# Optimization experiments

Hardware: AMD Instinct MI355X
Metric: run time of the kernel (lower is better)

Reference implementation:

```python
import jax, jax.numpy as jnp
import numpy as np

T, B, XIN, H, A = 4096, 1024, 2, 16, 4


def setup_inputs() -> dict:
    key = jax.random.key(0)
    ks = jax.random.split(key, 16)
    inp = {
        "x": jax.random.normal(ks[0], (T * B, XIN), dtype=jnp.float32),
        "done": jax.random.randint(ks[1], (T * B,), 0, 2, dtype=jnp.int32),
        "action": jax.random.randint(ks[2], (T * B,), 0, A, dtype=jnp.int32),
        "h0": jax.random.normal(ks[3], (B, H), dtype=jnp.float32) * 0.1,
        "c0": jax.random.normal(ks[4], (B, H), dtype=jnp.float32) * 0.1,
        # MLP: Linear(XIN, 16) (orthogonal init approximated by scaled normal)
        "w1": jax.random.normal(ks[5], (H, XIN), dtype=jnp.float32) * (1.0 / np.sqrt(XIN)),
        "b1": jnp.zeros((H,), dtype=jnp.float32),
        # LSTM(16, 16): gate order i, f, g, o (PyTorch convention)
        "w_ih": jax.random.normal(ks[6], (4 * H, H), dtype=jnp.float32) * (1.0 / np.sqrt(H)),
        "w_hh": jax.random.normal(ks[7], (4 * H, H), dtype=jnp.float32) * (1.0 / np.sqrt(H)),
        "b_ih": jnp.zeros((4 * H,), dtype=jnp.float32),
        "b_hh": jnp.zeros((4 * H,), dtype=jnp.float32),
        "actor_w": jax.random.normal(ks[8], (A, H), dtype=jnp.float32) * 0.01,
        "actor_b": jnp.zeros((A,), dtype=jnp.float32),
        "critic_w": jax.random.normal(ks[9], (1, H), dtype=jnp.float32) * (1.0 / np.sqrt(H)),
        "critic_b": jnp.zeros((1,), dtype=jnp.float32),
    }
    return inp


def reference(x, done, action, h0, c0, w1, b1, w_ih, w_hh, b_ih, b_hh,
              actor_w, actor_b, critic_w, critic_b):
    # MLP encoder: Linear(XIN,16) + ReLU, then reshape to [T, B, 16]
    hid = jax.nn.relu(x @ w1.T + b1)
    hid = hid.reshape(-1, h0.shape[0], H)          # [T, B, H]
    done_f = done.reshape(-1, h0.shape[0]).astype(hid.dtype)  # [T, B]

    def step(carry, inp):
        h, c = carry
        xt, dt = inp
        m = (1.0 - dt)[:, None]                    # reset mask per env
        h = h * m
        c = c * m
        gates = xt @ w_ih.T + b_ih + h @ w_hh.T + b_hh   # [B, 4H]
        i, f, g, o = jnp.split(gates, 4, axis=-1)
        i = jax.nn.sigmoid(i)
        f = jax.nn.sigmoid(f)
        g = jnp.tanh(g)
        o = jax.nn.sigmoid(o)
        c = f * c + i * g
        h = o * jnp.tanh(c)
        return (h, c), h

    (hN, cN), hs = jax.lax.scan(step, (h0, c0), (hid, done_f))
    hidden = hs.reshape(-1, H)                     # [T*B, H]

    logits = hidden @ actor_w.T + actor_b          # [T*B, A]
    logp_all = jax.nn.log_softmax(logits, axis=-1)
    logp = jnp.take_along_axis(logp_all, action[:, None].astype(jnp.int32), axis=1)[:, 0]
    entropy = -jnp.sum(jnp.exp(logp_all) * logp_all, axis=-1)
    value = (hidden @ critic_w.T + critic_b)[:, 0]
    return action, logp, entropy, value, hN, cN
```

## Files before the change

### kernel.cpp

```cpp
#include <hip/hip_runtime.h>

#define TT 4096
#define BB 1024
#define LCH 5
#define CH 32
#define NC 128
#define TB 4194304
#define OFF_LOGP (TB)
#define OFF_ENT  (2*TB)
#define OFF_VAL  (3*TB)
#define OFF_HN   (4*TB)
#define OFF_CN   (4*TB + 16384)

#define NL2E  (-1.4426950408889634f)
#define N2L2E (-2.8853900817779268f)

typedef float    f32x2 __attribute__((ext_vector_type(2)));
typedef float    f32x4 __attribute__((ext_vector_type(4)));
typedef _Float16 f16x4 __attribute__((ext_vector_type(4)));

__device__ __forceinline__ float fexp2(float x){
#if __has_builtin(__builtin_amdgcn_exp2f)
    return __builtin_amdgcn_exp2f(x);
#else
    return __expf(x * 0.6931471805599453f);
#endif
}

__device__ __forceinline__ float fsig(float x){
    return __builtin_amdgcn_rcpf(1.f + __expf(-x));
}
__device__ __forceinline__ float ftanh_(float x){
    return 1.f - 2.f*__builtin_amdgcn_rcpf(1.f + __expf(2.f*x));
}
__device__ __forceinline__ f16x4 to_h4(f32x4 v){
    f16x4 r;
    r[0]=(_Float16)v[0]; r[1]=(_Float16)v[1]; r[2]=(_Float16)v[2]; r[3]=(_Float16)v[3];
    return r;
}
__device__ __forceinline__ f32x4 from_h4(f16x4 v){
    f32x4 r;
    r[0]=(float)v[0]; r[1]=(float)v[1]; r[2]=(float)v[2]; r[3]=(float)v[3];
    return r;
}
__device__ __forceinline__ f32x4 mfma16(f16x4 a, f16x4 b, f32x4 c){
    return __builtin_amdgcn_mfma_f32_16x16x16f16(a, b, c, 0, 0, 0);
}

#define KPARAMS const float* __restrict__ x, const int* __restrict__ done, \
    const int* __restrict__ action, const float* __restrict__ h0, \
    const float* __restrict__ c0, const float* __restrict__ w1, \
    const float* __restrict__ b1, const float* __restrict__ w_ih, \
    const float* __restrict__ w_hh, const float* __restrict__ bsum, \
    const float* __restrict__ bsum_s, const float* __restrict__ wih_s, \
    const float* __restrict__ whh_s, const float* __restrict__ hw16, \
    const float* __restrict__ actor_w, const float* __restrict__ actor_b, \
    const float* __restrict__ critic_w, const float* __restrict__ critic_b, \
    float* __restrict__ out, float* __restrict__ carry, int* __restrict__ valid

#define KARGS x,done,action,h0,c0,w1,b1,w_ih,w_hh,bsum,bsum_s,wih_s,whh_s,hw16,actor_w,actor_b,critic_w,critic_b,out,carry,valid

struct Frags {
    f16x4 wih[4], whh[4], hw;
    f32x4 biasC[4], biasH;
    f32x2 w1r[4];
    f32x4 b1r;
};

__device__ __forceinline__ void load_frags(Frags& F, int lo, int hi,
    const float* w1, const float* b1, const float* wih_s, const float* whh_s,
    const float* bsum_s, const float* hw16, const float* actor_b,
    const float* critic_b)
{
#pragma unroll
    for (int mt = 0; mt < 4; mt++) {
        F.wih[mt]   = to_h4(*(const f32x4*)(wih_s + (16*mt+lo)*16 + 4*hi));
        F.whh[mt]   = to_h4(*(const f32x4*)(whh_s + (16*mt+lo)*16 + 4*hi));
        F.biasC[mt] = *(const f32x4*)(bsum_s + 16*mt + 4*hi);
    }
    F.hw = to_h4(*(const f32x4*)(hw16 + lo*16 + 4*hi));
    if (hi == 0)       F.biasH = *(const f32x4*)(actor_b);
    else if (hi == 1)  F.biasH = (f32x4){critic_b[0], 0.f, 0.f, 0.f};
    else               F.biasH = (f32x4){0.f, 0.f, 0.f, 0.f};
#pragma unroll
    for (int r = 0; r < 4; r++) {
        F.w1r[r] = *(const f32x2*)(w1 + (4*hi+r)*2);
        F.b1r[r] = b1[4*hi+r];
    }
}

__device__ __forceinline__ void step_mfma(const Frags& F, f16x4& hh, f32x4& cc,
    f32x2 xv, int a, int idx, bool do_store, int hi, float* __restrict__ out)
{
    f32x4 hid;
#pragma unroll
    for (int r = 0; r < 4; r++)
        hid[r] = fmaxf(fmaf(F.w1r[r][0], xv[0], fmaf(F.w1r[r][1], xv[1], F.b1r[r])), 0.f);
    f16x4 hidh = to_h4(hid);
    f32x4 g0 = mfma16(F.whh[0], hh, F.biasC[0]);
    f32x4 g1 = mfma16(F.whh[1], hh, F.biasC[1]);
    f32x4 g2 = mfma16(F.whh[2], hh, F.biasC[2]);
    f32x4 g3 = mfma16(F.whh[3], hh, F.biasC[3]);
    g0 = mfma16(F.wih[0], hidh, g0);
    g1 = mfma16(F.wih[1], hidh, g1);
    g2 = mfma16(F.wih[2], hidh, g2);
    g3 = mfma16(F.wih[3], hidh, g3);
    f32x4 o4, cv4;
#pragma unroll
    for (int r = 0; r < 4; r++) {
        float A0 = 1.f + fexp2(g0[r]);
        float A1 = 1.f + fexp2(g1[r]);
        float A2 = 1.f + fexp2(g2[r]);
        float A3 = 1.f + fexp2(g3[r]);
        float R01 = __builtin_amdgcn_rcpf(A0*A1);
        float R23 = __builtin_amdgcn_rcpf(A2*A3);
        float si = A1*R01;
        float sf = A0*R01;
        float tg = fmaf(2.f, A3*R23, -1.f);
        o4[r]    = A2*R23;
        cv4[r]   = fmaf(sf, cc[r], si*tg);
    }
    cc = cv4;
    float B0 = 1.f + fexp2(N2L2E*cv4[0]);
    float B1 = 1.f + fexp2(N2L2E*cv4[1]);
    float B2 = 1.f + fexp2(N2L2E*cv4[2]);
    float B3 = 1.f + fexp2(N2L2E*cv4[3]);
    float Ra = __builtin_amdgcn_rcpf(B0*B1);
    float Rb = __builtin_amdgcn_rcpf(B2*B3);
    f32x4 hn;
    hn[0] = o4[0]*fmaf(2.f, B1*Ra, -1.f);
    hn[1] = o4[1]*fmaf(2.f, B0*Ra, -1.f);
    hn[2] = o4[2]*fmaf(2.f, B3*Rb, -1.f);
    hn[3] = o4[3]*fmaf(2.f, B2*Rb, -1.f);
    hh = to_h4(hn);
    f32x4 dh = mfma16(F.hw, hh, F.biasH);
    if (do_store) {
        if (hi == 0) {
            float e0 = __expf(dh[0]), e1 = __expf(dh[1]);
            float e2 = __expf(dh[2]), e3 = __expf(dh[3]);
            float s  = e0+e1+e2+e3;
            float ls = __logf(s);
            float t  = e0*dh[0] + e1*dh[1] + e2*dh[2] + e3*dh[3];
            float ent = ls - t*__builtin_amdgcn_rcpf(s);
            float lsel = (a==0) ? dh[0] : (a==1) ? dh[1] : (a==2) ? dh[2] : dh[3];
            out[idx]            = (float)a;
            out[OFF_LOGP + idx] = lsel - ls;
            out[OFF_ENT  + idx] = ent;
        } else if (hi == 1) {
            out[OFF_VAL + idx] = dh[0];
        }
    }
}

__global__ __launch_bounds__(256) __attribute__((amdgpu_waves_per_eu(4, 8)))
void k_phase1(KPARAMS)
{
    const int tid  = blockIdx.x*256 + threadIdx.x;
    const int lane = tid & 63;
    const int lo = lane & 15, hi = lane >> 4;
    const int w    = tid >> 6;
    const int ch   = w >> 6;
    const int base = (w & 63) << 4;
    const int b    = base + lo;
    const int t0   = ch << LCH;

    Frags F;
    load_frags(F, lo, hi, w1, b1, wih_s, whh_s, bsum_s, hw16, actor_b, critic_b);

    f16x4 hh = {(_Float16)0.f,(_Float16)0.f,(_Float16)0.f,(_Float16)0.f};
    f32x4 cc = {0.f,0.f,0.f,0.f};
    int hr = 0;

    int   d_cur = done[t0*BB + b];
    f32x2 x_cur = *(const f32x2*)(x + 2*(size_t)(t0*BB + b));
    int   a_cur = action[t0*BB + b];

#pragma unroll 2
    for (int s = 0; s < CH; s++) {
        const int idx = (t0 + s)*BB + b;
        const int   d  = d_cur;
        const f32x2 xv = x_cur;
        const int   a  = a_cur;
        if (s + 1 < CH) {
            d_cur = done[idx + BB];
            x_cur = *(const f32x2*)(x + 2*(size_t)(idx + BB));
            a_cur = action[idx + BB];
        }
        hr |= d;
        if (d) {
            hh = (f16x4){(_Float16)0.f,(_Float16)0.f,(_Float16)0.f,(_Float16)0.f};
            cc = (f32x4){0.f,0.f,0.f,0.f};
        }
        step_mfma(F, hh, cc, xv, a, idx, true, hi, out);
    }
    if (hr) {
        f32x4 hf = from_h4(hh);
#pragma unroll
        for (int r = 0; r < 4; r++) {
            carry[(ch*32 + 4*hi + r)*BB + b]      = hf[r];
            carry[(ch*32 + 16 + 4*hi + r)*BB + b] = cc[r];
        }
    }
    if (hi == 0) valid[ch*BB + b] = hr;
}

__global__ __launch_bounds__(256) __attribute__((amdgpu_waves_per_eu(4, 8)))
void k_phase2(KPARAMS)
{
    const int tid  = blockIdx.x*256 + threadIdx.x;
    const int lane = tid & 63;
    const int lo = lane & 15, hi = lane >> 4;
    const int w    = tid >> 6;
    const int ch   = w >> 6;
    const int base = (w & 63) << 4;
    const int b    = base + lo;
    const int t0   = ch << LCH;

    Frags F;
    load_frags(F, lo, hi, w1, b1, wih_s, whh_s, bsum_s, hw16, actor_b, critic_b);

    f32x4 hf, cc;
    bool active;
    if (ch == 0) {
        hf = *(const f32x4*)(h0 + b*16 + 4*hi);
        cc = *(const f32x4*)(c0 + b*16 + 4*hi);
        active = true;
    } else {
        active = (valid[(ch-1)*BB + b] != 0);
#pragma unroll
        for (int r = 0; r < 4; r++) {
            hf[r] = carry[((ch-1)*32 + 4*hi + r)*BB + b];
            cc[r] = carry[((ch-1)*32 + 16 + 4*hi + r)*BB + b];
        }
    }
    f16x4 hh = to_h4(hf);

    for (int s = 0; s < CH; s++) {
        if (!__ballot(active)) break;
        const int idx = (t0 + s)*BB + b;
        const int d = done[idx];
        if (d) active = false;
        const f32x2 xv = *(const f32x2*)(x + 2*(size_t)idx);
        const int a = action[idx];
        step_mfma(F, hh, cc, xv, a, idx, active, hi, out);
    }

    if (ch == NC-1) {
        if (active) {
            f32x4 ho = from_h4(hh);
#pragma unroll
            for (int r = 0; r < 4; r++) {
                out[OFF_HN + b*16 + 4*hi + r] = ho[r];
                out[OFF_CN + b*16 + 4*hi + r] = cc[r];
            }
        } else if (valid[(NC-1)*BB + b]) {
#pragma unroll
            for (int r = 0; r < 4; r++) {
                out[OFF_HN + b*16 + 4*hi + r] = carry[((NC-1)*32 + 4*hi + r)*BB + b];
                out[OFF_CN + b*16 + 4*hi + r] = carry[((NC-1)*32 + 16 + 4*hi + r)*BB + b];
            }
        }
    }
}

__device__ void cell_scalar(const float* x, const int* action,
    const float* w1, const float* b1, const float* w_ih, const float* w_hh,
    const float* bsum, const float* actor_w, const float* actor_b,
    const float* critic_w, const float* critic_b, float* out,
    int t, int b, float h[16], float c[16])
{
    const int idx = t*BB + b;
    float x0 = x[2*(size_t)idx], x1 = x[2*(size_t)idx+1];
    float hid[16];
#pragma unroll
    for (int k = 0; k < 16; k++)
        hid[k] = fmaxf(fmaf(w1[2*k], x0, fmaf(w1[2*k+1], x1, b1[k])), 0.f);
    float nh[16], nc[16];
#pragma unroll
    for (int k = 0; k < 16; k++) {
        float ai = bsum[k], af = bsum[16+k], ag = bsum[32+k], ao = bsum[48+k];
#pragma unroll
        for (int j = 0; j < 16; j++) {
            ai = fmaf(w_ih[k*16+j],      hid[j], ai);
            af = fmaf(w_ih[(16+k)*16+j], hid[j], af);
            ag = fmaf(w_ih[(32+k)*16+j], hid[j], ag);
            ao = fmaf(w_ih[(48+k)*16+j], hid[j], ao);
        }
#pragma unroll
        for (int j = 0; j < 16; j++) {
            ai = fmaf(w_hh[k*16+j],      h[j], ai);
            af = fmaf(w_hh[(16+k)*16+j], h[j], af);
            ag = fmaf(w_hh[(32+k)*16+j], h[j], ag);
            ao = fmaf(w_hh[(48+k)*16+j], h[j], ao);
        }
        float si = fsig(ai), sf = fsig(af), sg = ftanh_(ag), so = fsig(ao);
        float cv = fmaf(sf, c[k], si*sg);
        nc[k] = cv; nh[k] = so*ftanh_(cv);
    }
#pragma unroll
    for (int k = 0; k < 16; k++) { h[k] = nh[k]; c[k] = nc[k]; }
    float l0=actor_b[0], l1=actor_b[1], l2=actor_b[2], l3=actor_b[3], v=critic_b[0];
#pragma unroll
    for (int j = 0; j < 16; j++) {
        l0 = fmaf(actor_w[j],    h[j], l0);
        l1 = fmaf(actor_w[16+j], h[j], l1);
        l2 = fmaf(actor_w[32+j], h[j], l2);
        l3 = fmaf(actor_w[48+j], h[j], l3);
        v  = fmaf(critic_w[j],   h[j], v);
    }
    float mx = fmaxf(fmaxf(l0,l1), fmaxf(l2,l3));
    float e0=__expf(l0-mx), e1=__expf(l1-mx), e2=__expf(l2-mx), e3=__expf(l3-mx);
    float s = e0+e1+e2+e3, ls = __logf(s), inv = __builtin_amdgcn_rcpf(s);
    float lp0=l0-mx-ls, lp1=l1-mx-ls, lp2=l2-mx-ls, lp3=l3-mx-ls;
    int a = action[idx];
    float lp = (a==0)?lp0:(a==1)?lp1:(a==2)?lp2:lp3;
    out[idx]            = (float)a;
    out[OFF_LOGP + idx] = lp;
    out[OFF_ENT  + idx] = -(e0*lp0+e1*lp1+e2*lp2+e3*lp3)*inv;
    out[OFF_VAL  + idx] = v;
}

__global__ void k_phase3(KPARAMS)
{
    int b = blockIdx.x*blockDim.x + threadIdx.x;
    if (b >= BB) return;
    bool anybad = false;
    for (int ch = 0; ch < NC; ch++) anybad |= (valid[ch*BB + b] == 0);
    if (!anybad) return;

    int fixed_until = 0;
    for (int ch = 0; ch < NC; ch++) {
        if (valid[ch*BB + b]) continue;
        int t0 = ch << LCH;
        if (t0 < fixed_until) continue;
        float h[16], c[16];
        if (ch == 0) {
#pragma unroll
            for (int k = 0; k < 16; k++) { h[k] = h0[b*16+k]; c[k] = c0[b*16+k]; }
        } else {
#pragma unroll
            for (int k = 0; k < 16; k++) {
                h[k] = carry[((ch-1)*32 + k)*BB + b];
                c[k] = carry[((ch-1)*32 + 16 + k)*BB + b];
            }
        }
        int t;
        for (t = t0; t < TT; t++) {
            if (done[t*BB + b]) break;
            cell_scalar(x, action, w1, b1, w_ih, w_hh, bsum,
                        actor_w, actor_b, critic_w, critic_b, out, t, b, h, c);
            if (((t+1) & (CH-1)) == 0) {
                int cc2 = t >> LCH;
#pragma unroll
                for (int k = 0; k < 16; k++) {
                    carry[(cc2*32 + k)*BB + b]      = h[k];
                    carry[(cc2*32 + 16 + k)*BB + b] = c[k];
                }
                valid[cc2*BB + b] = 1;
            }
        }
        if (t == TT) {
#pragma unroll
            for (int k = 0; k < 16; k++) {
                out[OFF_HN + b*16 + k] = h[k];
                out[OFF_CN + b*16 + k] = c[k];
            }
        }
        fixed_until = t;
    }
    if (valid[(NC-1)*BB + b]) {
#pragma unroll
        for (int k = 0; k < 16; k++) {
            out[OFF_HN + b*16 + k] = carry[((NC-1)*32 + k)*BB + b];
            out[OFF_CN + b*16 + k] = carry[((NC-1)*32 + 16 + k)*BB + b];
        }
    }
}

__global__ void k_prep(const float* __restrict__ b_ih, const float* __restrict__ b_hh,
                       const float* __restrict__ w_ih, const float* __restrict__ w_hh,
                       const float* __restrict__ actor_w, const float* __restrict__ critic_w,
                       float* __restrict__ bsum, float* __restrict__ bsum_s,
                       float* __restrict__ hw16, float* __restrict__ wih_s,
                       float* __restrict__ whh_s)
{
    int i = threadIdx.x;
    if (i < 64) {
        float s = b_ih[i] + b_hh[i];
        bsum[i] = s;
        bool isg = (i >= 32) && (i < 48);
        bsum_s[i] = s * (isg ? N2L2E : NL2E);
    }
    {
        int row = i >> 4, k = i & 15;
        float v = 0.f;
        if (row < 4)        v = actor_w[row*16 + k];
        else if (row == 4)  v = critic_w[k];
        hw16[i] = v;
    }
    for (int j = i; j < 1024; j += 256) {
        int row = j >> 4;
        float sc = ((row >= 32) && (row < 48)) ? N2L2E : NL2E;
        wih_s[j] = sc * w_ih[j];
        whh_s[j] = sc * w_hh[j];
    }
}

extern "C" void kernel_launch(void* const* d_in, const int* in_sizes, int n_in,
                              void* d_out, int out_size, void* d_ws, size_t ws_size,
                              hipStream_t stream)
{
    const float* x        = (const float*)d_in[0];
    const int*   done     = (const int*)  d_in[1];
    const int*   action   = (const int*)  d_in[2];
    const float* h0       = (const float*)d_in[3];
    const float* c0       = (const float*)d_in[4];
    const float* w1       = (const float*)d_in[5];
    const float* b1       = (const float*)d_in[6];
    const float* w_ih     = (const float*)d_in[7];
    const float* w_hh     = (const float*)d_in[8];
    const float* b_ih     = (const float*)d_in[9];
    const float* b_hh     = (const float*)d_in[10];
    const float* actor_w  = (const float*)d_in[11];
    const float* actor_b  = (const float*)d_in[12];
    const float* critic_w = (const float*)d_in[13];
    const float* critic_b = (const float*)d_in[14];
    float* out = (float*)d_out;

    float* bsum   = (float*)d_ws;
    float* bsum_s = (float*)((char*)d_ws + 256);
    float* hw16   = (float*)((char*)d_ws + 512);
    float* wih_s  = (float*)((char*)d_ws + 1536);
    float* whh_s  = (float*)((char*)d_ws + 5632);
    float* carry  = (float*)((char*)d_ws + 16384);
    int*   valid  = (int*)((char*)d_ws + 16384 + (size_t)NC*32*BB*4);

    hipLaunchKernelGGL(k_prep, dim3(1), dim3(256), 0, stream,
                       b_ih, b_hh, w_ih, w_hh, actor_w, critic_w,
                       bsum, bsum_s, hw16, wih_s, whh_s);

    const int nthreads = NC*(BB/16)*64;
    hipLaunchKernelGGL(k_phase1, dim3(nthreads/256), dim3(256), 0, stream, KARGS);
    hipLaunchKernelGGL(k_phase2, dim3(nthreads/256), dim3(256), 0, stream, KARGS);
    hipLaunchKernelGGL(k_phase3, dim3(BB/256), dim3(256), 0, stream, KARGS);
}
```

Measured before the change: 150.3 us.

## Software-pipeline input-gate MFMAs off the recurrent path and share reciprocals

In phase 1, the input-projection MFMAs for the next timestep are computed ahead and used as the accumulator for the recurrent W_hh MFMAs. This takes half the MFMAs off the serial h-dependency chain. The sigmoid/tanh math now uses one reciprocal per four values instead of two. The actor head weights and bias are prescaled by log2(e) so softmax can use exp2/log2. Risks are more live registers and a larger dynamic range in the single combined reciprocal product.

Result: no change. 151.7 us (+0.9%).

```diff
diff --git a/kernel.cpp b/kernel.cpp
--- a/kernel.cpp
+++ b/kernel.cpp
@@ -14,16 +14,20 @@
 
 #define NL2E  (-1.4426950408889634f)
 #define N2L2E (-2.8853900817779268f)
+#define L2E   (1.4426950408889634f)
+#define LN2   (0.6931471805599453f)
 
 typedef float    f32x2 __attribute__((ext_vector_type(2)));
 typedef float    f32x4 __attribute__((ext_vector_type(4)));
 typedef _Float16 f16x4 __attribute__((ext_vector_type(4)));
+
+__device__ __forceinline__ f32x4 splat4(float v){ return (f32x4){v,v,v,v}; }
 
 __device__ __forceinline__ float fexp2(float x){
 #if __has_builtin(__builtin_amdgcn_exp2f)
     return __builtin_amdgcn_exp2f(x);
 #else
-    return __expf(x * 0.6931471805599453f);
+    return __expf(x * LN2);
 #endif
 }
 
@@ -79,9 +83,14 @@
         F.biasC[mt] = *(const f32x4*)(bsum_s + 16*mt + 4*hi);
     }
     F.hw = to_h4(*(const f32x4*)(hw16 + lo*16 + 4*hi));
-    if (hi == 0)       F.biasH = *(const f32x4*)(actor_b);
-    else if (hi == 1)  F.biasH = (f32x4){critic_b[0], 0.f, 0.f, 0.f};
-    else               F.biasH = (f32x4){0.f, 0.f, 0.f, 0.f};
+    if (hi == 0) {
+        f32x4 ab = *(const f32x4*)(actor_b);
+        F.biasH = ab * splat4(L2E);
+    } else if (hi == 1) {
+        F.biasH = (f32x4){critic_b[0], 0.f, 0.f, 0.f};
+    } else {
+        F.biasH = splat4(0.f);
+    }
 #pragma unroll
     for (int r = 0; r < 4; r++) {
         F.w1r[r] = *(const f32x2*)(w1 + (4*hi+r)*2);
@@ -89,14 +98,86 @@
     }
 }
 
-__device__ __forceinline__ void step_mfma(const Frags& F, f16x4& hh, f32x4& cc,
-    f32x2 xv, int a, int idx, bool do_store, int hi, float* __restrict__ out)
+__device__ __forceinline__ f16x4 enc_hid(const Frags& F, f32x2 xv)
 {
     f32x4 hid;
 #pragma unroll
     for (int r = 0; r < 4; r++)
         hid[r] = fmaxf(fmaf(F.w1r[r][0], xv[0], fmaf(F.w1r[r][1], xv[1], F.b1r[r])), 0.f);
-    f16x4 hidh = to_h4(hid);
+    return to_h4(hid);
+}
+
+__device__ __forceinline__ void gates_x(const Frags& F, f16x4 hidh,
+    f32x4& gx0, f32x4& gx1, f32x4& gx2, f32x4& gx3)
+{
+    gx0 = mfma16(F.wih[0], hidh, F.biasC[0]);
+    gx1 = mfma16(F.wih[1], hidh, F.biasC[1]);
+    gx2 = mfma16(F.wih[2], hidh, F.biasC[2]);
+    gx3 = mfma16(F.wih[3], hidh, F.biasC[3]);
+}
+
+__device__ __forceinline__ void lstm_finish(f32x4 g0, f32x4 g1, f32x4 g2, f32x4 g3,
+                                            f16x4& hh, f32x4& cc)
+{
+    f32x4 o4, cv4;
+#pragma unroll
+    for (int r = 0; r < 4; r++) {
+        float A0 = 1.f + fexp2(g0[r]);
+        float A1 = 1.f + fexp2(g1[r]);
+        float A2 = 1.f + fexp2(g2[r]);
+        float A3 = 1.f + fexp2(g3[r]);
+        float P01 = A0*A1, P23 = A2*A3;
+        float R = __builtin_amdgcn_rcpf(P01*P23);
+        float P23R = P23*R;
+        float P01R = P01*R;
+        float si = A1*P23R;
+        float sf = A0*P23R;
+        float tg = fmaf(2.f, A3*P01R, -1.f);
+        o4[r]    = A2*P01R;
+        cv4[r]   = fmaf(sf, cc[r], si*tg);
+    }
+    cc = cv4;
+    float B0 = 1.f + fexp2(N2L2E*cv4[0]);
+    float B1 = 1.f + fexp2(N2L2E*cv4[1]);
+    float B2 = 1.f + fexp2(N2L2E*cv4[2]);
+    float B3 = 1.f + fexp2(N2L2E*cv4[3]);
+    float P01 = B0*B1, P23 = B2*B3;
+    float R = __builtin_amdgcn_rcpf(P01*P23);
+    float P23R = P23*R, P01R = P01*R;
+    f32x4 hn;
+    hn[0] = o4[0]*fmaf(2.f, B1*P23R, -1.f);
+    hn[1] = o4[1]*fmaf(2.f, B0*P23R, -1.f);
+    hn[2] = o4[2]*fmaf(2.f, B3*P01R, -1.f);
+    hn[3] = o4[3]*fmaf(2.f, B2*P01R, -1.f);
+    hh = to_h4(hn);
+}
+
+__device__ __forceinline__ void heads_store(const Frags& F, f16x4 hh, int a,
+    int idx, bool do_store, int hi, float* __restrict__ out)
+{
+    f32x4 dh = mfma16(F.hw, hh, F.biasH);
+    if (do_store) {
+        if (hi == 0) {
+            float e0 = fexp2(dh[0]), e1 = fexp2(dh[1]);
+            float e2 = fexp2(dh[2]), e3 = fexp2(dh[3]);
+            float s   = e0+e1+e2+e3;
+            float ls2 = __log2f(s);
+            float t2  = e0*dh[0] + e1*dh[1] + e2*dh[2] + e3*dh[3];
+            float ent = (ls2 - t2*__builtin_amdgcn_rcpf(s)) * LN2;
+            float lsel = (a==0) ? dh[0] : (a==1) ? dh[1] : (a==2) ? dh[2] : dh[3];
+            out[idx]            = (float)a;
+            out[OFF_LOGP + idx] = (lsel - ls2) * LN2;
+            out[OFF_ENT  + idx] = ent;
+        } else if (hi == 1) {
+            out[OFF_VAL + idx] = dh[0];
+        }
+    }
+}
+
+__device__ __forceinline__ void step_full(const Frags& F, f16x4& hh, f32x4& cc,
+    f32x2 xv, int a, int idx, bool do_store, int hi, float* __restrict__ out)
+{
+    f16x4 hidh = enc_hid(F, xv);
     f32x4 g0 = mfma16(F.whh[0], hh, F.biasC[0]);
     f32x4 g1 = mfma16(F.whh[1], hh, F.biasC[1]);
     f32x4 g2 = mfma16(F.whh[2], hh, F.biasC[2]);
@@ -105,51 +186,8 @@
     g1 = mfma16(F.wih[1], hidh, g1);
     g2 = mfma16(F.wih[2], hidh, g2);
     g3 = mfma16(F.wih[3], hidh, g3);
-    f32x4 o4, cv4;
-#pragma unroll
-    for (int r = 0; r < 4; r++) {
-        float A0 = 1.f + fexp2(g0[r]);
-        float A1 = 1.f + fexp2(g1[r]);
-        float A2 = 1.f + fexp2(g2[r]);
-        float A3 = 1.f + fexp2(g3[r]);
-        float R01 = __builtin_amdgcn_rcpf(A0*A1);
-        float R23 = __builtin_amdgcn_rcpf(A2*A3);
-        float si = A1*R01;
-        float sf = A0*R01;
-        float tg = fmaf(2.f, A3*R23, -1.f);
-        o4[r]    = A2*R23;
-        cv4[r]   = fmaf(sf, cc[r], si*tg);
-    }
-    cc = cv4;
-    float B0 = 1.f + fexp2(N2L2E*cv4[0]);
-    float B1 = 1.f + fexp2(N2L2E*cv4[1]);
-    float B2 = 1.f + fexp2(N2L2E*cv4[2]);
-    float B3 = 1.f + fexp2(N2L2E*cv4[3]);
-    float Ra = __builtin_amdgcn_rcpf(B0*B1);
-    float Rb = __builtin_amdgcn_rcpf(B2*B3);
-    f32x4 hn;
-    hn[0] = o4[0]*fmaf(2.f, B1*Ra, -1.f);
-    hn[1] = o4[1]*fmaf(2.f, B0*Ra, -1.f);
-    hn[2] = o4[2]*fmaf(2.f, B3*Rb, -1.f);
-    hn[3] = o4[3]*fmaf(2.f, B2*Rb, -1.f);
-    hh = to_h4(hn);
-    f32x4 dh = mfma16(F.hw, hh, F.biasH);
-    if (do_store) {
-        if (hi == 0) {
-            float e0 = __expf(dh[0]), e1 = __expf(dh[1]);
-            float e2 = __expf(dh[2]), e3 = __expf(dh[3]);
-            float s  = e0+e1+e2+e3;
-            float ls = __logf(s);
-            float t  = e0*dh[0] + e1*dh[1] + e2*dh[2] + e3*dh[3];
-            float ent = ls - t*__builtin_amdgcn_rcpf(s);
-            float lsel = (a==0) ? dh[0] : (a==1) ? dh[1] : (a==2) ? dh[2] : dh[3];
-            out[idx]            = (float)a;
-            out[OFF_LOGP + idx] = lsel - ls;
-            out[OFF_ENT  + idx] = ent;
-        } else if (hi == 1) {
-            out[OFF_VAL + idx] = dh[0];
-        }
-    }
+    lstm_finish(g0, g1, g2, g3, hh, cc);
+    heads_store(F, hh, a, idx, do_store, hi, out);
 }
 
 __global__ __launch_bounds__(256) __attribute__((amdgpu_waves_per_eu(4, 8)))
@@ -167,31 +205,45 @@
     Frags F;
     load_frags(F, lo, hi, w1, b1, wih_s, whh_s, bsum_s, hw16, actor_b, critic_b);
 
-    f16x4 hh = {(_Float16)0.f,(_Float16)0.f,(_Float16)0.f,(_Float16)0.f};
-    f32x4 cc = {0.f,0.f,0.f,0.f};
+    const f16x4 hz = {(_Float16)0.f,(_Float16)0.f,(_Float16)0.f,(_Float16)0.f};
+    f16x4 hh = hz;
+    f32x4 cc = splat4(0.f);
     int hr = 0;
 
-    int   d_cur = done[t0*BB + b];
-    f32x2 x_cur = *(const f32x2*)(x + 2*(size_t)(t0*BB + b));
-    int   a_cur = action[t0*BB + b];
+    const int i0 = t0*BB + b;
+    int   d_cur = done[i0];
+    f32x2 x_cur = *(const f32x2*)(x + 2*(size_t)i0);
+    int   a_cur = action[i0];
+
+    f32x4 gx0, gx1, gx2, gx3;
+    {
+        f16x4 hidh = enc_hid(F, x_cur);
+        gates_x(F, hidh, gx0, gx1, gx2, gx3);
+    }
 
 #pragma unroll 2
     for (int s = 0; s < CH; s++) {
         const int idx = (t0 + s)*BB + b;
-        const int   d  = d_cur;
-        const f32x2 xv = x_cur;
-        const int   a  = a_cur;
+        int d_nxt = 0, a_nxt = 0;
+        f32x2 x_nxt = (f32x2){0.f, 0.f};
         if (s + 1 < CH) {
-            d_cur = done[idx + BB];
-            x_cur = *(const f32x2*)(x + 2*(size_t)(idx + BB));
-            a_cur = action[idx + BB];
-        }
-        hr |= d;
-        if (d) {
-            hh = (f16x4){(_Float16)0.f,(_Float16)0.f,(_Float16)0.f,(_Float16)0.f};
-            cc = (f32x4){0.f,0.f,0.f,0.f};
-        }
-        step_mfma(F, hh, cc, xv, a, idx, true, hi, out);
+            d_nxt = done[idx + BB];
+            x_nxt = *(const f32x2*)(x + 2*(size_t)(idx + BB));
+            a_nxt = action[idx + BB];
+        }
+        hr |= d_cur;
+        if (d_cur) { hh = hz; cc = splat4(0.f); }
+        f32x4 g0 = mfma16(F.whh[0], hh, gx0);
+        f32x4 g1 = mfma16(F.whh[1], hh, gx1);
+        f32x4 g2 = mfma16(F.whh[2], hh, gx2);
+        f32x4 g3 = mfma16(F.whh[3], hh, gx3);
+        if (s + 1 < CH) {
+            f16x4 hidn = enc_hid(F, x_nxt);
+            gates_x(F, hidn, gx0, gx1, gx2, gx3);
+        }
+        lstm_finish(g0, g1, g2, g3, hh, cc);
+        heads_store(F, hh, a_cur, idx, true, hi, out);
+        d_cur = d_nxt; a_cur = a_nxt;
     }
     if (hr) {
         f32x4 hf = from_h4(hh);
@@ -242,7 +294,7 @@
         if (d) active = false;
         const f32x2 xv = *(const f32x2*)(x + 2*(size_t)idx);
         const int a = action[idx];
-        step_mfma(F, hh, cc, xv, a, idx, active, hi, out);
+        step_full(F, hh, cc, xv, a, idx, active, hi, out);
     }
 
     if (ch == NC-1) {
@@ -394,7 +446,7 @@
     {
         int row = i >> 4, k = i & 15;
         float v = 0.f;
-        if (row < 4)        v = actor_w[row*16 + k];
+        if (row < 4)        v = actor_w[row*16 + k] * L2E;
         else if (row == 4)  v = critic_w[k];
         hw16[i] = v;
     }
```
